# Kernel optimization log

Measured on AMD Instinct MI355X. Metric: run time of the kernel, lower is better.

## Reference

```python
import jax, jax.numpy as jnp
import numpy as np
import math

B = 16
D = 1024
K = 64
ALPHA = 0.0
N_MAX = 8192


def setup_inputs() -> dict:
    key = jax.random.key(0)
    k1, k2 = jax.random.split(key)
    lengths = jax.random.randint(k1, (B,), N_MAX // 2, N_MAX + 1)
    lengths = lengths.at[0].set(N_MAX)  # ensure max(lengths) == N_MAX, matching torch N_max
    lengths = lengths.astype(jnp.int64) if jax.config.jax_enable_x64 else lengths.astype(jnp.int32)
    W = jax.random.normal(k2, (D, 2 * K), dtype=jnp.float32) * (1.0 / math.sqrt(2 * K))
    return {"lengths": lengths, "W": W, "N_max": N_MAX}


def reference(lengths, W, N_max):
    # lengths: [B] int, W: [d, 2K] (torch Linear weight), N_max: python int
    d, twoK = W.shape
    Kk = twoK // 2
    k = jnp.arange(1, Kk + 1, dtype=jnp.float32)                      # [K]
    Delta = 2.0 * math.pi * k[None, :] / lengths[:, None].astype(jnp.float32)  # [B, K]
    t = jnp.arange(N_max, dtype=jnp.float32)                          # [N]
    theta = t[None, :, None] * Delta[:, None, :]                      # [B, N, K] closed-form angle
    amp = (k ** (-ALPHA)) * (1.0 / math.sqrt(Kk))                     # [K]
    # interleave (cos, sin) pairs along last dim: [c1,s1,c2,s2,...]
    cs = jnp.stack([jnp.cos(theta), jnp.sin(theta)], axis=-1)         # [B, N, K, 2]
    feats = (cs * amp[None, None, :, None]).reshape(theta.shape[0], N_max, twoK)
    mask = jnp.arange(N_max)[None, :] < lengths[:, None]              # [B, N]
    feats = feats * mask[:, :, None].astype(feats.dtype)
    pos_emb = jnp.einsum('bnf,df->bnd', feats, W)                     # [B, N, d]
    return pos_emb, mask
```

## Files before the change

### kernel.cpp

```cpp
#include <hip/hip_runtime.h>
#include <math.h>

#define B_DIM    16
#define D_DIM    1024
#define K_FREQ   64
#define F_DIM    128
#define N_MAXLEN 8192

#define BM   128
#define BN   128
#define LDSS 136

typedef __attribute__((ext_vector_type(8))) short bf16x8;
typedef __attribute__((ext_vector_type(4))) float f32x4;

__device__ __forceinline__ unsigned short f2bf(float x) {
    union { float f; unsigned u; } v; v.f = x;
    unsigned r = (v.u + 0x7FFFu + ((v.u >> 16) & 1u)) >> 16;
    return (unsigned short)r;
}

__global__ __launch_bounds__(256, 2) void cyclic_gemm_kernel(
    const int* __restrict__ lengths,
    const float* __restrict__ W,
    float* __restrict__ out)
{
    __shared__ short sA[BM * LDSS];
    __shared__ short sB[BN * LDSS];

    const int tid = threadIdx.x;
    const int m0  = blockIdx.y * BM;
    const int d0  = blockIdx.x * BN;

    {
        const int r    = tid >> 1;
        const int half = tid & 1;
        const int m    = m0 + r;
        const int b    = m >> 13;
        const int n    = m & (N_MAXLEN - 1);
        const int len  = lengths[b];
        unsigned* dst = (unsigned*)&sA[r * LDSS + half * 64];
        if (n >= len) {
            #pragma unroll
            for (int j = 0; j < 32; ++j) dst[j] = 0u;
        } else {
            const float base = (float)n / (float)len;
            #pragma unroll
            for (int j = 0; j < 32; ++j) {
                const int k = half * 32 + j;
                float rev = base * (float)(k + 1);
                rev -= floorf(rev);
                float s, c;
                __sincosf(6.283185307179586f * rev, &s, &c);
                const unsigned cb = f2bf(c * 0.125f);
                const unsigned sb = f2bf(s * 0.125f);
                dst[j] = cb | (sb << 16);
            }
        }
    }

    {
        const float4* Wv = (const float4*)(W + (size_t)d0 * F_DIM);
        #pragma unroll
        for (int i = 0; i < 16; ++i) {
            const int lin = tid + i * 256;
            const int row = lin >> 5;
            const int c4  = lin & 31;
            const float4 w = Wv[row * 32 + c4];
            unsigned* p = (unsigned*)&sB[row * LDSS + c4 * 4];
            p[0] = (unsigned)f2bf(w.x) | ((unsigned)f2bf(w.y) << 16);
            p[1] = (unsigned)f2bf(w.z) | ((unsigned)f2bf(w.w) << 16);
        }
    }

    __syncthreads();

    const int lane = tid & 63;
    const int wave = tid >> 6;
    const int wm   = (wave >> 1) * 64;
    const int wn   = (wave & 1) * 64;
    const int lrow = lane & 15;
    const int quad = lane >> 4;

    f32x4 acc[4][4];
    #pragma unroll
    for (int mi = 0; mi < 4; ++mi)
        #pragma unroll
        for (int ni = 0; ni < 4; ++ni)
            acc[mi][ni] = (f32x4){0.f, 0.f, 0.f, 0.f};

    const short* aBase = &sA[(wm + lrow) * LDSS + quad * 8];
    const short* bBase = &sB[(wn + lrow) * LDSS + quad * 8];

    #pragma unroll
    for (int ks = 0; ks < 4; ++ks) {
        bf16x8 af[4], bfr[4];
        #pragma unroll
        for (int i = 0; i < 4; ++i) {
            af[i]  = *(const bf16x8*)(aBase + i * 16 * LDSS + ks * 32);
            bfr[i] = *(const bf16x8*)(bBase + i * 16 * LDSS + ks * 32);
        }
        #pragma unroll
        for (int mi = 0; mi < 4; ++mi)
            #pragma unroll
            for (int ni = 0; ni < 4; ++ni)
                acc[mi][ni] = __builtin_amdgcn_mfma_f32_16x16x32_bf16(
                    af[mi], bfr[ni], acc[mi][ni], 0, 0, 0);
    }

    #pragma unroll
    for (int mi = 0; mi < 4; ++mi) {
        #pragma unroll
        for (int reg = 0; reg < 4; ++reg) {
            const int row = m0 + wm + mi * 16 + quad * 4 + reg;
            float* orow = out + (size_t)row * D_DIM + (d0 + wn + lrow);
            #pragma unroll
            for (int ni = 0; ni < 4; ++ni)
                orow[ni * 16] = acc[mi][ni][reg];
        }
    }
}

__global__ void mask_kernel(const int* __restrict__ lengths, float* __restrict__ maskp) {
    const int i = blockIdx.x * blockDim.x + threadIdx.x;
    const int b = i >> 13;
    const int n = i & (N_MAXLEN - 1);
    maskp[i] = (n < lengths[b]) ? 1.0f : 0.0f;
}

extern "C" void kernel_launch(void* const* d_in, const int* in_sizes, int n_in,
                              void* d_out, int out_size, void* d_ws, size_t ws_size,
                              hipStream_t stream) {
    const int*   lengths = (const int*)d_in[0];
    const float* W       = (const float*)d_in[1];
    float* out   = (float*)d_out;
    float* maskp = out + (size_t)B_DIM * N_MAXLEN * D_DIM;

    dim3 grid(D_DIM / BN, (B_DIM * N_MAXLEN) / BM);
    cyclic_gemm_kernel<<<grid, dim3(256), 0, stream>>>(lengths, W, out);

    const int mtot = B_DIM * N_MAXLEN;
    mask_kernel<<<mtot / 256, dim3(256), 0, stream>>>(lengths, maskp);
}
```

Measured before the change: 520.0 us.

## Keep sinusoid features in registers and sweep all D tiles per row block

Each block now owns 128 rows and loops over all eight 128-wide output-column tiles. The cosine/sine features are computed once per row block straight into MFMA A-fragment registers instead of being recomputed for every column tile. W is converted to padded bf16 once in a prep kernel that also writes the mask, and each tile is then streamed into LDS with global_load_lds. Row blocks that lie entirely past the sequence length skip the GEMM and write zeros with vectorised stores. The trade-off is less grid parallelism (one block per row block) and serialised LDS reloads between tiles, each fenced by two barriers.

```diff
diff --git a/kernel.cpp b/kernel.cpp
--- a/kernel.cpp
+++ b/kernel.cpp
@@ -8,124 +8,162 @@
 #define N_MAXLEN 8192
 
 #define BM   128
-#define BN   128
 #define LDSS 136
+#define TILE_SHORTS (128 * LDSS)
 
 typedef __attribute__((ext_vector_type(8))) short bf16x8;
 typedef __attribute__((ext_vector_type(4))) float f32x4;
 
-__device__ __forceinline__ unsigned short f2bf(float x) {
+__device__ __forceinline__ unsigned f2bf(float x) {
     union { float f; unsigned u; } v; v.f = x;
-    unsigned r = (v.u + 0x7FFFu + ((v.u >> 16) & 1u)) >> 16;
-    return (unsigned short)r;
+    return (v.u + 0x7FFFu + ((v.u >> 16) & 1u)) >> 16;
 }
 
-__global__ __launch_bounds__(256, 2) void cyclic_gemm_kernel(
+__device__ __forceinline__ void gload_lds16(const void* g, void* l) {
+    __builtin_amdgcn_global_load_lds(
+        (const __attribute__((address_space(1))) void*)g,
+        (__attribute__((address_space(3))) void*)l, 16, 0, 0);
+}
+
+__global__ __launch_bounds__(256) void prep_kernel(
     const int* __restrict__ lengths,
     const float* __restrict__ W,
+    short* __restrict__ Wb,
+    float* __restrict__ maskp)
+{
+    const int i = blockIdx.x * 256 + threadIdx.x;
+    const float4 w = ((const float4*)W)[i];
+    const int row = i >> 5;
+    const int c4  = i & 31;
+    unsigned* p = (unsigned*)&Wb[row * LDSS + c4 * 4];
+    p[0] = f2bf(w.x) | (f2bf(w.y) << 16);
+    p[1] = f2bf(w.z) | (f2bf(w.w) << 16);
+
+    const int m4  = i << 2;
+    const int b   = m4 >> 13;
+    const int n   = m4 & (N_MAXLEN - 1);
+    const int len = lengths[b];
+    float4 mv;
+    mv.x = (n     < len) ? 1.f : 0.f;
+    mv.y = (n + 1 < len) ? 1.f : 0.f;
+    mv.z = (n + 2 < len) ? 1.f : 0.f;
+    mv.w = (n + 3 < len) ? 1.f : 0.f;
+    ((float4*)maskp)[i] = mv;
+}
+
+__global__ __launch_bounds__(256, 3) void cyclic_gemm_kernel(
+    const int* __restrict__ lengths,
+    const short* __restrict__ Wb,
     float* __restrict__ out)
 {
-    __shared__ short sA[BM * LDSS];
-    __shared__ short sB[BN * LDSS];
+    __shared__ short sB[TILE_SHORTS];
 
-    const int tid = threadIdx.x;
-    const int m0  = blockIdx.y * BM;
-    const int d0  = blockIdx.x * BN;
+    const int tid  = threadIdx.x;
+    const int lane = tid & 63;
+    const int wave = tid >> 6;
+    const int lrow = lane & 15;
+    const int quad = lane >> 4;
+    const int m0   = blockIdx.x * BM;
+    const int b    = m0 >> 13;
+    const int n0   = m0 & (N_MAXLEN - 1);
+    const int len  = lengths[b];
+
+    if (n0 >= len) {
+        const float4 z = {0.f, 0.f, 0.f, 0.f};
+        float4* p = (float4*)(out + (size_t)m0 * D_DIM);
+        #pragma unroll 8
+        for (int i = tid; i < BM * D_DIM / 4; i += 256) p[i] = z;
+        return;
+    }
 
     {
-        const int r    = tid >> 1;
-        const int half = tid & 1;
-        const int m    = m0 + r;
-        const int b    = m >> 13;
-        const int n    = m & (N_MAXLEN - 1);
-        const int len  = lengths[b];
-        unsigned* dst = (unsigned*)&sA[r * LDSS + half * 64];
+        const short* Wt = Wb;
+        #pragma unroll
+        for (int i = 0; i < 8; ++i) {
+            const int cb = i * 256 + wave * 64;
+            gload_lds16(Wt + (size_t)(cb + lane) * 8, sB + (size_t)cb * 8);
+        }
+        if (wave < 2) {
+            const int cb = 2048 + wave * 64;
+            gload_lds16(Wt + (size_t)(cb + lane) * 8, sB + (size_t)cb * 8);
+        }
+    }
+
+    bf16x8 af[2][4];
+    #pragma unroll
+    for (int mi = 0; mi < 2; ++mi) {
+        const int n = n0 + wave * 32 + mi * 16 + lrow;
         if (n >= len) {
             #pragma unroll
-            for (int j = 0; j < 32; ++j) dst[j] = 0u;
+            for (int ks = 0; ks < 4; ++ks)
+                af[mi][ks] = (bf16x8){0,0,0,0,0,0,0,0};
         } else {
             const float base = (float)n / (float)len;
             #pragma unroll
-            for (int j = 0; j < 32; ++j) {
-                const int k = half * 32 + j;
-                float rev = base * (float)(k + 1);
-                rev -= floorf(rev);
-                float s, c;
-                __sincosf(6.283185307179586f * rev, &s, &c);
-                const unsigned cb = f2bf(c * 0.125f);
-                const unsigned sb = f2bf(s * 0.125f);
-                dst[j] = cb | (sb << 16);
+            for (int ks = 0; ks < 4; ++ks) {
+                #pragma unroll
+                for (int jj = 0; jj < 4; ++jj) {
+                    const int k = ks * 16 + quad * 4 + jj;
+                    float rev = base * (float)(k + 1);
+                    rev -= floorf(rev);
+                    float s, c;
+                    __sincosf(6.283185307179586f * rev, &s, &c);
+                    af[mi][ks][2*jj]     = (short)f2bf(c * 0.125f);
+                    af[mi][ks][2*jj + 1] = (short)f2bf(s * 0.125f);
+                }
             }
         }
     }
 
-    {
-        const float4* Wv = (const float4*)(W + (size_t)d0 * F_DIM);
+    #pragma unroll 1
+    for (int t = 0; t < 8; ++t) {
+        __syncthreads();
+
+        f32x4 acc[2][8];
         #pragma unroll
-        for (int i = 0; i < 16; ++i) {
-            const int lin = tid + i * 256;
-            const int row = lin >> 5;
-            const int c4  = lin & 31;
-            const float4 w = Wv[row * 32 + c4];
-            unsigned* p = (unsigned*)&sB[row * LDSS + c4 * 4];
-            p[0] = (unsigned)f2bf(w.x) | ((unsigned)f2bf(w.y) << 16);
-            p[1] = (unsigned)f2bf(w.z) | ((unsigned)f2bf(w.w) << 16);
+        for (int mi = 0; mi < 2; ++mi)
+            #pragma unroll
+            for (int ni = 0; ni < 8; ++ni)
+                acc[mi][ni] = (f32x4){0.f, 0.f, 0.f, 0.f};
+
+        #pragma unroll
+        for (int ks = 0; ks < 4; ++ks) {
+            bf16x8 bfr[8];
+            #pragma unroll
+            for (int ni = 0; ni < 8; ++ni)
+                bfr[ni] = *(const bf16x8*)&sB[(ni*16 + lrow) * LDSS + ks*32 + quad*8];
+            #pragma unroll
+            for (int mi = 0; mi < 2; ++mi)
+                #pragma unroll
+                for (int ni = 0; ni < 8; ++ni)
+                    acc[mi][ni] = __builtin_amdgcn_mfma_f32_16x16x32_bf16(
+                        bfr[ni], af[mi][ks], acc[mi][ni], 0, 0, 0);
+        }
+
+        if (t < 7) {
+            __syncthreads();
+            const short* Wt = Wb + (size_t)(t + 1) * TILE_SHORTS;
+            #pragma unroll
+            for (int i = 0; i < 8; ++i) {
+                const int cb = i * 256 + wave * 64;
+                gload_lds16(Wt + (size_t)(cb + lane) * 8, sB + (size_t)cb * 8);
+            }
+            if (wave < 2) {
+                const int cb = 2048 + wave * 64;
+                gload_lds16(Wt + (size_t)(cb + lane) * 8, sB + (size_t)cb * 8);
+            }
+        }
+
+        const int d0 = t * 128;
+        #pragma unroll
+        for (int mi = 0; mi < 2; ++mi) {
+            const int m = m0 + wave * 32 + mi * 16 + lrow;
+            float* orow = out + (size_t)m * D_DIM + d0 + quad * 4;
+            #pragma unroll
+            for (int ni = 0; ni < 8; ++ni)
+                *(float4*)(orow + ni * 16) = *(float4*)&acc[mi][ni];
         }
     }
-
-    __syncthreads();
-
-    const int lane = tid & 63;
-    const int wave = tid >> 6;
-    const int wm   = (wave >> 1) * 64;
-    const int wn   = (wave & 1) * 64;
-    const int lrow = lane & 15;
-    const int quad = lane >> 4;
-
-    f32x4 acc[4][4];
-    #pragma unroll
-    for (int mi = 0; mi < 4; ++mi)
-        #pragma unroll
-        for (int ni = 0; ni < 4; ++ni)
-            acc[mi][ni] = (f32x4){0.f, 0.f, 0.f, 0.f};
-
-    const short* aBase = &sA[(wm + lrow) * LDSS + quad * 8];
-    const short* bBase = &sB[(wn + lrow) * LDSS + quad * 8];
-
-    #pragma unroll
-    for (int ks = 0; ks < 4; ++ks) {
-        bf16x8 af[4], bfr[4];
-        #pragma unroll
-        for (int i = 0; i < 4; ++i) {
-            af[i]  = *(const bf16x8*)(aBase + i * 16 * LDSS + ks * 32);
-            bfr[i] = *(const bf16x8*)(bBase + i * 16 * LDSS + ks * 32);
-        }
-        #pragma unroll
-        for (int mi = 0; mi < 4; ++mi)
-            #pragma unroll
-            for (int ni = 0; ni < 4; ++ni)
-                acc[mi][ni] = __builtin_amdgcn_mfma_f32_16x16x32_bf16(
-                    af[mi], bfr[ni], acc[mi][ni], 0, 0, 0);
-    }
-
-    #pragma unroll
-    for (int mi = 0; mi < 4; ++mi) {
-        #pragma unroll
-        for (int reg = 0; reg < 4; ++reg) {
-            const int row = m0 + wm + mi * 16 + quad * 4 + reg;
-            float* orow = out + (size_t)row * D_DIM + (d0 + wn + lrow);
-            #pragma unroll
-            for (int ni = 0; ni < 4; ++ni)
-                orow[ni * 16] = acc[mi][ni][reg];
-        }
-    }
-}
-
-__global__ void mask_kernel(const int* __restrict__ lengths, float* __restrict__ maskp) {
-    const int i = blockIdx.x * blockDim.x + threadIdx.x;
-    const int b = i >> 13;
-    const int n = i & (N_MAXLEN - 1);
-    maskp[i] = (n < lengths[b]) ? 1.0f : 0.0f;
 }
 
 extern "C" void kernel_launch(void* const* d_in, const int* in_sizes, int n_in,
@@ -135,10 +173,10 @@
     const float* W       = (const float*)d_in[1];
     float* out   = (float*)d_out;
     float* maskp = out + (size_t)B_DIM * N_MAXLEN * D_DIM;
+    short* Wb    = (short*)d_ws;
 
-    dim3 grid(D_DIM / BN, (B_DIM * N_MAXLEN) / BM);
-    cyclic_gemm_kernel<<<grid, dim3(256), 0, stream>>>(lengths, W, out);
+    prep_kernel<<<dim3(128), dim3(256), 0, stream>>>(lengths, W, Wb, maskp);
 
-    const int mtot = B_DIM * N_MAXLEN;
-    mask_kernel<<<mtot / 256, dim3(256), 0, stream>>>(lengths, maskp);
+    dim3 grid((B_DIM * N_MAXLEN) / BM);
+    cyclic_gemm_kernel<<<grid, dim3(256), 0, stream>>>(lengths, Wb, out);
 }
```

Measured after the change: 545.5 us. +4.9%, slower.

## Precompute bf16 features and weights once; skip GEMM for fully masked tiles

Applied to the files above, without the earlier changes.

Cyclic features and the bf16-converted W are now built once by separate prep kernels into a padded workspace layout. Before, each GEMM block recomputed sincos and converted W per tile, so the same work was repeated across every d-tile. The GEMM now fills LDS with direct global-to-LDS loads, and blocks whose whole row range lies beyond the sequence length just write zeros. The mask write is folded into the W prep kernel. This adds two extra launches and a roughly 35 MB intermediate buffer, and if the workspace is too small it falls back to a buffer placed past the mask output, which could write out of bounds.

```diff
diff --git a/kernel.cpp b/kernel.cpp
--- a/kernel.cpp
+++ b/kernel.cpp
@@ -10,69 +10,121 @@
 #define BM   128
 #define BN   128
 #define LDSS 136
+#define TILE_SHORTS (128 * LDSS)
+#define A_CHUNKS 2176
+#define ALL_CHUNKS (2 * A_CHUNKS)
 
 typedef __attribute__((ext_vector_type(8))) short bf16x8;
 typedef __attribute__((ext_vector_type(4))) float f32x4;
 
-__device__ __forceinline__ unsigned short f2bf(float x) {
+__device__ __forceinline__ unsigned f2bf(float x) {
     union { float f; unsigned u; } v; v.f = x;
-    unsigned r = (v.u + 0x7FFFu + ((v.u >> 16) & 1u)) >> 16;
-    return (unsigned short)r;
+    return (v.u + 0x7FFFu + ((v.u >> 16) & 1u)) >> 16;
+}
+
+__device__ __forceinline__ void gload_lds16(const void* g, void* l) {
+    __builtin_amdgcn_global_load_lds(
+        (const __attribute__((address_space(1))) void*)g,
+        (__attribute__((address_space(3))) void*)l, 16, 0, 0);
+}
+
+__global__ __launch_bounds__(256) void prep_w_kernel(
+    const int* __restrict__ lengths,
+    const float* __restrict__ W,
+    short* __restrict__ Wb,
+    float* __restrict__ maskp)
+{
+    const int i = blockIdx.x * 256 + threadIdx.x;
+    const float4 w = ((const float4*)W)[i];
+    const int row = i >> 5;
+    const int c4  = i & 31;
+    uint2 packed;
+    packed.x = f2bf(w.x) | (f2bf(w.y) << 16);
+    packed.y = f2bf(w.z) | (f2bf(w.w) << 16);
+    *(uint2*)&Wb[(size_t)row * LDSS + c4 * 4] = packed;
+
+    const int m4  = i << 2;
+    const int b   = m4 >> 13;
+    const int n   = m4 & (N_MAXLEN - 1);
+    const int len = lengths[b];
+    float4 mv;
+    mv.x = (n     < len) ? 1.f : 0.f;
+    mv.y = (n + 1 < len) ? 1.f : 0.f;
+    mv.z = (n + 2 < len) ? 1.f : 0.f;
+    mv.w = (n + 3 < len) ? 1.f : 0.f;
+    ((float4*)maskp)[i] = mv;
+}
+
+__global__ __launch_bounds__(256) void feats_kernel(
+    const int* __restrict__ lengths,
+    short* __restrict__ Wf)
+{
+    const int g    = blockIdx.x * 256 + threadIdx.x;
+    const int m    = g >> 1;
+    const int half = g & 1;
+    const int b    = m >> 13;
+    const int n    = m & (N_MAXLEN - 1);
+    const int len  = lengths[b];
+
+    unsigned vals[32];
+    if (n >= len) {
+        #pragma unroll
+        for (int j = 0; j < 32; ++j) vals[j] = 0u;
+    } else {
+        const float base = (float)n / (float)len;
+        #pragma unroll
+        for (int j = 0; j < 32; ++j) {
+            const int k = half * 32 + j;
+            float rev = base * (float)(k + 1);
+            rev -= floorf(rev);
+            float s, c;
+            __sincosf(6.283185307179586f * rev, &s, &c);
+            vals[j] = f2bf(c * 0.125f) | (f2bf(s * 0.125f) << 16);
+        }
+    }
+    uint4* dst = (uint4*)&Wf[(size_t)m * LDSS + half * 64];
+    #pragma unroll
+    for (int i = 0; i < 8; ++i)
+        dst[i] = (uint4){vals[4*i], vals[4*i+1], vals[4*i+2], vals[4*i+3]};
 }
 
 __global__ __launch_bounds__(256, 2) void cyclic_gemm_kernel(
     const int* __restrict__ lengths,
-    const float* __restrict__ W,
+    const short* __restrict__ Wb,
+    const short* __restrict__ Wf,
     float* __restrict__ out)
 {
-    __shared__ short sA[BM * LDSS];
-    __shared__ short sB[BN * LDSS];
+    __shared__ short s[2 * TILE_SHORTS];
 
     const int tid = threadIdx.x;
-    const int m0  = blockIdx.y * BM;
-    const int d0  = blockIdx.x * BN;
+    const int m0  = blockIdx.x * BM;
+    const int d0  = blockIdx.y * BN;
+    const int b   = m0 >> 13;
+    const int n0  = m0 & (N_MAXLEN - 1);
+    const int len = lengths[b];
 
-    {
-        const int r    = tid >> 1;
-        const int half = tid & 1;
-        const int m    = m0 + r;
-        const int b    = m >> 13;
-        const int n    = m & (N_MAXLEN - 1);
-        const int len  = lengths[b];
-        unsigned* dst = (unsigned*)&sA[r * LDSS + half * 64];
-        if (n >= len) {
-            #pragma unroll
-            for (int j = 0; j < 32; ++j) dst[j] = 0u;
-        } else {
-            const float base = (float)n / (float)len;
-            #pragma unroll
-            for (int j = 0; j < 32; ++j) {
-                const int k = half * 32 + j;
-                float rev = base * (float)(k + 1);
-                rev -= floorf(rev);
-                float s, c;
-                __sincosf(6.283185307179586f * rev, &s, &c);
-                const unsigned cb = f2bf(c * 0.125f);
-                const unsigned sb = f2bf(s * 0.125f);
-                dst[j] = cb | (sb << 16);
-            }
+    if (n0 >= len) {
+        const float4 z = {0.f, 0.f, 0.f, 0.f};
+        #pragma unroll 4
+        for (int i = tid; i < BM * BN / 4; i += 256) {
+            const int r = i >> 5;
+            const int c = i & 31;
+            *(float4*)(out + (size_t)(m0 + r) * D_DIM + d0 + c * 4) = z;
         }
+        return;
     }
 
     {
-        const float4* Wv = (const float4*)(W + (size_t)d0 * F_DIM);
+        const short* Af = Wf + (size_t)m0 * LDSS;
+        const short* Bf = Wb + (size_t)d0 * LDSS;
         #pragma unroll
-        for (int i = 0; i < 16; ++i) {
-            const int lin = tid + i * 256;
-            const int row = lin >> 5;
-            const int c4  = lin & 31;
-            const float4 w = Wv[row * 32 + c4];
-            unsigned* p = (unsigned*)&sB[row * LDSS + c4 * 4];
-            p[0] = (unsigned)f2bf(w.x) | ((unsigned)f2bf(w.y) << 16);
-            p[1] = (unsigned)f2bf(w.z) | ((unsigned)f2bf(w.w) << 16);
+        for (int i = 0; i < 17; ++i) {
+            const int chunk = i * 256 + tid;
+            const short* src = (chunk < A_CHUNKS) ? (Af + (size_t)chunk * 8)
+                                                  : (Bf + (size_t)(chunk - A_CHUNKS) * 8);
+            gload_lds16(src, s + (size_t)chunk * 8);
         }
     }
-
     __syncthreads();
 
     const int lane = tid & 63;
@@ -89,8 +141,8 @@
         for (int ni = 0; ni < 4; ++ni)
             acc[mi][ni] = (f32x4){0.f, 0.f, 0.f, 0.f};
 
-    const short* aBase = &sA[(wm + lrow) * LDSS + quad * 8];
-    const short* bBase = &sB[(wn + lrow) * LDSS + quad * 8];
+    const short* aBase = &s[(wm + lrow) * LDSS + quad * 8];
+    const short* bBase = &s[TILE_SHORTS + (wn + lrow) * LDSS + quad * 8];
 
     #pragma unroll
     for (int ks = 0; ks < 4; ++ks) {
@@ -121,13 +173,6 @@
     }
 }
 
-__global__ void mask_kernel(const int* __restrict__ lengths, float* __restrict__ maskp) {
-    const int i = blockIdx.x * blockDim.x + threadIdx.x;
-    const int b = i >> 13;
-    const int n = i & (N_MAXLEN - 1);
-    maskp[i] = (n < lengths[b]) ? 1.0f : 0.0f;
-}
-
 extern "C" void kernel_launch(void* const* d_in, const int* in_sizes, int n_in,
                               void* d_out, int out_size, void* d_ws, size_t ws_size,
                               hipStream_t stream) {
@@ -136,9 +181,19 @@
     float* out   = (float*)d_out;
     float* maskp = out + (size_t)B_DIM * N_MAXLEN * D_DIM;
 
-    dim3 grid(D_DIM / BN, (B_DIM * N_MAXLEN) / BM);
-    cyclic_gemm_kernel<<<grid, dim3(256), 0, stream>>>(lengths, W, out);
+    const size_t wb_bytes = (size_t)D_DIM * LDSS * sizeof(short);
+    const size_t wf_bytes = (size_t)B_DIM * N_MAXLEN * LDSS * sizeof(short);
+    short* Wb;
+    if (ws_size >= wb_bytes + wf_bytes) {
+        Wb = (short*)d_ws;
+    } else {
+        Wb = (short*)(maskp + (size_t)B_DIM * N_MAXLEN);
+    }
+    short* Wf = Wb + (size_t)D_DIM * LDSS;
 
-    const int mtot = B_DIM * N_MAXLEN;
-    mask_kernel<<<mtot / 256, dim3(256), 0, stream>>>(lengths, maskp);
+    prep_w_kernel<<<dim3(128), dim3(256), 0, stream>>>(lengths, W, Wb, maskp);
+    feats_kernel<<<dim3((B_DIM * N_MAXLEN * 2) / 256), dim3(256), 0, stream>>>(lengths, Wf);
+
+    dim3 grid((B_DIM * N_MAXLEN) / BM, D_DIM / BN);
+    cyclic_gemm_kernel<<<grid, dim3(256), 0, stream>>>(lengths, Wb, Wf, out);
 }
```

Measured after the change: 594.7 us. 14.4% more time.
